# Optimization experiments

Hardware: AMD Instinct MI355X
Metric: run time of the kernel (lower is better)

## Reference

```python
import jax, jax.numpy as jnp
import numpy as np

B, N, DIN, U, K, DEG = 64, 512, 256, 128, 2, 8
BN = B * N
E = BN * DEG
D4 = 4 * U
HEADS = 2


def setup_inputs() -> dict:
    key = jax.random.key(0)
    ks = jax.random.split(key, 24)
    rng = np.random.default_rng(0)
    # block-diagonal batched graph: each of B graphs has N nodes, N*DEG random edges
    src = rng.integers(0, N, size=(B, N * DEG))
    dst = rng.integers(0, N, size=(B, N * DEG))
    off = (np.arange(B) * N)[:, None]
    edge_index = jnp.asarray(np.stack([(src + off).reshape(-1), (dst + off).reshape(-1)]), dtype=jnp.int32)

    def w(k, shape, fan):
        return (jax.random.normal(k, shape, dtype=jnp.float32) / np.sqrt(fan)).astype(jnp.float32)

    gin = (DIN + U) * (K + 1)  # gconv concatenates K+1 hop features of concat([x, h])
    inp = dict(
        x_od=jax.random.normal(ks[0], (BN, DIN), dtype=jnp.float32),
        history=jax.random.normal(ks[1], (BN, DIN), dtype=jnp.float32),
        yesterday=jax.random.normal(ks[2], (BN, DIN), dtype=jnp.float32),
        edge_index=edge_index,
        edge_weight=jax.random.uniform(ks[3], (E,), dtype=jnp.float32),
        W_ru_f=w(ks[4], (gin, 2 * U), gin), b_ru_f=jnp.zeros((2 * U,), jnp.float32),
        W_c_f=w(ks[5], (gin, U), gin), b_c_f=jnp.zeros((U,), jnp.float32),
        W_ru_l=w(ks[6], (gin, 2 * U), gin), b_ru_l=jnp.zeros((2 * U,), jnp.float32),
        W_c_l=w(ks[7], (gin, U), gin), b_c_l=jnp.zeros((U,), jnp.float32),
        W_ru_s=w(ks[8], (gin, 2 * U), gin), b_ru_s=jnp.zeros((2 * U,), jnp.float32),
        W_c_s=w(ks[9], (gin, U), gin), b_c_s=jnp.zeros((U,), jnp.float32),
        W_hd=w(ks[10], (D4, 2 * U), 2 * U), b_hd=jnp.zeros((D4,), jnp.float32),
        W_in=w(ks[11], (3 * D4, D4), D4), b_in=jnp.zeros((3 * D4,), jnp.float32),
        W_out=w(ks[12], (D4, D4), D4), b_out=jnp.zeros((D4,), jnp.float32),
        W_gate=w(ks[13], (U, D4), D4), b_gate=jnp.zeros((U,), jnp.float32),
    )
    return inp


def _gconv(x, src, dst, ew, W, b):
    # K-hop mean-normalized graph convolution over the batched edge list
    num = x.shape[0]
    deg = jnp.maximum(jax.ops.segment_sum(ew, dst, num_segments=num), 1.0)[:, None]
    feats = [x]
    h = x
    for _ in range(K):
        h = jax.ops.segment_sum(h[src] * ew[:, None], dst, num_segments=num) / deg
        feats.append(h)
    return jnp.concatenate(feats, axis=-1) @ W + b


def _ggru(x, h, src, dst, ew, W_ru, b_ru, W_c, b_c):
    ru = jax.nn.sigmoid(_gconv(jnp.concatenate([x, h], -1), src, dst, ew, W_ru, b_ru))
    r, u = jnp.split(ru, 2, axis=-1)
    c = jnp.tanh(_gconv(jnp.concatenate([x, r * h], -1), src, dst, ew, W_c, b_c))
    return u * h + (1.0 - u) * c


def _pos_enc(seq_len, d):
    pos = jnp.arange(seq_len, dtype=jnp.float32)[:, None]
    div = jnp.exp(jnp.arange(0, d, 2, dtype=jnp.float32) * (-jnp.log(10000.0) / d))
    pe = jnp.zeros((seq_len, d), jnp.float32)
    pe = pe.at[:, 0::2].set(jnp.sin(pos * div)).at[:, 1::2].set(jnp.cos(pos * div))
    return pe  # (seq_len, d)


def reference(x_od, history, yesterday, edge_index, edge_weight,
              W_ru_f, b_ru_f, W_c_f, b_c_f,
              W_ru_l, b_ru_l, W_c_l, b_c_l,
              W_ru_s, b_ru_s, W_c_s, b_c_s,
              W_hd, b_hd, W_in, b_in, W_out, b_out, W_gate, b_gate):
    src, dst = edge_index[0], edge_index[1]
    ew = edge_weight
    h0 = jnp.zeros((BN, U), jnp.float32)
    hf = _ggru(x_od, h0, src, dst, ew, W_ru_f, b_ru_f, W_c_f, b_c_f)      # finished branch
    hl = _ggru(history, h0, src, dst, ew, W_ru_l, b_ru_l, W_c_l, b_c_l)  # long-history branch
    hs = _ggru(yesterday, h0, src, dst, ew, W_ru_s, b_ru_s, W_c_s, b_c_s)  # short-history branch
    # hidden fusion: raw view(-1, 2U, N) as in the torch source
    fusion = jnp.concatenate([hs, hl], axis=-1).reshape(B, 2 * U, N)
    uh = jnp.einsum('oc,bcn->bon', W_hd, fusion) + b_hd[:, None]  # (B, 4U, N)
    uh = uh + _pos_enc(B, D4)[:, :, None]                          # pos-enc over batch dim, as in source
    x = uh.transpose(2, 0, 1)                                      # (N, B, 4U): seq=N, batch=B
    # multi-head self-attention (torch MultiheadAttention semantics)
    qkv = x @ W_in.T + b_in
    q, k_, v = jnp.split(qkv, 3, axis=-1)
    hd = D4 // HEADS
    qh = q.reshape(N, B, HEADS, hd)
    kh = k_.reshape(N, B, HEADS, hd)
    vh = v.reshape(N, B, HEADS, hd)
    scores = jnp.einsum('sbhd,tbhd->bhst', qh, kh) / jnp.sqrt(jnp.float32(hd))
    attn = jax.nn.softmax(scores, axis=-1)
    ctx = jnp.einsum('bhst,tbhd->sbhd', attn, vh).reshape(N, B, D4)
    attn_out = ctx @ W_out.T + b_out                               # (N, B, 4U)
    gated = jnp.einsum('oc,bcn->bon', W_gate, attn_out.transpose(1, 2, 0)) + b_gate[:, None]  # (B, U, N)
    attn_flat = gated.transpose(0, 2, 1).reshape(BN, U)
    # (enc_first_out==finished_hidden, long_hidden, short_hidden, gated attention)
    return jnp.stack([hf, hl, hs, attn_flat])
```

## Files before the change

### kernel.cpp

```cpp
#include <hip/hip_runtime.h>
#include <hip/hip_bf16.h>
#include <math.h>


#define DEV __device__ __forceinline__

typedef __attribute__((ext_vector_type(4))) float  f32x4;
typedef __attribute__((ext_vector_type(4))) float  fvec4;
typedef __attribute__((ext_vector_type(8))) short  bf16x8;
typedef __attribute__((ext_vector_type(4))) unsigned short u16x4;

constexpr int BN_ = 32768;
constexpr int E_  = 262144;
constexpr long OUTSEC = 4194304;
constexpr long ZSZE = 25165824;

DEV unsigned short f2bf(float f){
  union { float f; unsigned u; } v; v.f = f;
  unsigned r = (v.u + 0x7FFFu + ((v.u >> 16) & 1u)) >> 16;
  return (unsigned short)r;
}
DEV float b2f(unsigned short h){
  union { unsigned u; float f; } v; v.u = ((unsigned)h) << 16;
  return v.f;
}

__global__ __launch_bounds__(256) void histdeg_kernel(const int* __restrict__ ei,
    const float* __restrict__ ew, unsigned* __restrict__ cnt, float* __restrict__ deg){
  int e = blockIdx.x*256 + threadIdx.x;
  int d = ei[E_ + e];
  atomicAdd(&cnt[d], 1u);
  atomicAdd(&deg[d], ew[e]);
}

__global__ __launch_bounds__(1024) void scan_kernel(const unsigned* __restrict__ cnt,
                                                    unsigned* __restrict__ rowptr){
  __shared__ unsigned sm[1024];
  __shared__ unsigned carry;
  int tid = threadIdx.x;
  if (tid == 0) carry = 0;
  __syncthreads();
  for (int base = 0; base < BN_; base += 1024){
    unsigned v = cnt[base + tid];
    sm[tid] = v;
    __syncthreads();
    for (int off = 1; off < 1024; off <<= 1){
      unsigned t = (tid >= off) ? sm[tid - off] : 0u;
      __syncthreads();
      sm[tid] += t;
      __syncthreads();
    }
    rowptr[base + tid] = carry + sm[tid] - v;
    __syncthreads();
    if (tid == 1023) carry += sm[1023];
    __syncthreads();
  }
  if (tid == 0) rowptr[BN_] = carry;
}

__global__ __launch_bounds__(256) void scatter_kernel(const int* __restrict__ ei,
    const float* __restrict__ ew, const unsigned* __restrict__ rowptr,
    unsigned* __restrict__ curs, unsigned* __restrict__ csrc, float* __restrict__ csrw){
  int e = blockIdx.x*256 + threadIdx.x;
  int d = ei[E_ + e];
  unsigned pos = atomicAdd(&curs[d], 1u);
  unsigned idx = rowptr[d] + pos;
  csrc[idx] = (unsigned)ei[e];
  csrw[idx] = ew[e];
}

template<int SRC>
__global__ __launch_bounds__(256) void prop3_kernel(const float* __restrict__ x0,
    const float* __restrict__ x1, const float* __restrict__ x2,
    unsigned short* __restrict__ zcat,
    const unsigned* __restrict__ rowptr, const unsigned* __restrict__ csrc,
    const float* __restrict__ csrw, const float* __restrict__ deg){
  int node = blockIdx.x*4 + (threadIdx.x >> 6);
  int l = threadIdx.x & 63;
  int z = blockIdx.z;
  const float* xf = (z == 0) ? x0 : (z == 1) ? x1 : x2;
  const unsigned short* zin = zcat + z*ZSZE + 256;
  unsigned short* zout = zcat + z*ZSZE + (SRC == 0 ? 256 : 512);
  unsigned b0 = rowptr[node], b1 = rowptr[node + 1];
  float a0 = 0.f, a1 = 0.f, a2 = 0.f, a3 = 0.f;
  for (unsigned e = b0; e < b1; ++e){
    int s = csrc[e]; float w = csrw[e];
    if constexpr (SRC == 0){
      fvec4 v = *(const fvec4*)(xf + (long)s*256 + l*4);
      a0 += w*v[0]; a1 += w*v[1]; a2 += w*v[2]; a3 += w*v[3];
    } else {
      u16x4 v = *(const u16x4*)(zin + (long)s*768 + l*4);
      a0 += w*b2f(v[0]); a1 += w*b2f(v[1]); a2 += w*b2f(v[2]); a3 += w*b2f(v[3]);
    }
  }
  float dg = deg[node]; dg = dg > 1.f ? dg : 1.f;
  float inv = 1.f / dg;
  u16x4 o = { f2bf(a0*inv), f2bf(a1*inv), f2bf(a2*inv), f2bf(a3*inv) };
  *(u16x4*)(zout + (long)node*768 + l*4) = o;
}

__global__ __launch_bounds__(256) void convx3_kernel(const float* __restrict__ x0,
    const float* __restrict__ x1, const float* __restrict__ x2,
    unsigned short* __restrict__ zcat){
  int id = blockIdx.x*256 + threadIdx.x;
  int z = blockIdx.z;
  const float* xf = (z == 0) ? x0 : (z == 1) ? x1 : x2;
  fvec4 v = ((const fvec4*)xf)[id];
  int m = id >> 6, c4 = id & 63;
  u16x4 o = { f2bf(v[0]), f2bf(v[1]), f2bf(v[2]), f2bf(v[3]) };
  *(u16x4*)(zcat + z*ZSZE + (long)m*768 + c4*4) = o;
}

__global__ __launch_bounds__(256) void cvt_f2b_kernel(const float* __restrict__ s,
                                                      unsigned short* __restrict__ d, int n){
  int i = blockIdx.x*256 + threadIdx.x;
  if (i < n) d[i] = f2bf(s[i]);
}

__global__ __launch_bounds__(256) void tcvt_kernel(const float* __restrict__ s,
    unsigned short* __restrict__ d, int lgC, int R){
  int id = blockIdx.x*256 + threadIdx.x;
  int r = id >> lgC, c = id & ((1 << lgC) - 1);
  d[(long)c*R + r] = f2bf(s[id]);
}

__global__ __launch_bounds__(256) void weff3_kernel(
    const float* __restrict__ Wru0, const float* __restrict__ Wru1, const float* __restrict__ Wru2,
    const float* __restrict__ bru0, const float* __restrict__ bru1, const float* __restrict__ bru2,
    const float* __restrict__ Wc0,  const float* __restrict__ Wc1,  const float* __restrict__ Wc2,
    const float* __restrict__ bc0,  const float* __restrict__ bc1,  const float* __restrict__ bc2,
    unsigned short* __restrict__ Weff, float* __restrict__ beff){
  int z = blockIdx.y;
  const float* Wru = (z == 0) ? Wru0 : (z == 1) ? Wru1 : Wru2;
  const float* bru = (z == 0) ? bru0 : (z == 1) ? bru1 : bru2;
  const float* Wc  = (z == 0) ? Wc0  : (z == 1) ? Wc1  : Wc2;
  const float* bc  = (z == 0) ? bc0  : (z == 1) ? bc1  : bc2;
  int id = blockIdx.x*256 + threadIdx.x;
  int n = id / 768, k = id % 768;
  int row = (k >> 8)*384 + (k & 255);
  int j = n >> 1;
  float w = ((n & 1) == 0) ? Wru[(long)row*256 + 128 + j] : Wc[(long)row*128 + j];
  Weff[(long)z*196608 + (long)n*768 + k] = f2bf(w);
  if (k == 0) beff[z*256 + n] = ((n & 1) == 0) ? bru[128 + j] : bc[j];
}

__global__ __launch_bounds__(256) void pe_kernel(const float* __restrict__ bhd,
                                                 float* __restrict__ PET4){
  int id = blockIdx.x*256 + threadIdx.x;
  int b = id >> 9, o = id & 511;
  float j2 = (float)(o & ~1);
  float ang = (float)b * expf(-j2 * (9.210340371976184f / 512.f));
  float v = ((o & 1) ? cosf(ang) : sinf(ang)) + bhd[o];
  PET4[(o >> 2)*256 + b*4 + (o & 3)] = v;
}

__global__ __launch_bounds__(256) void peq2_kernel(const float* __restrict__ Win,
    const float* __restrict__ bin, const float* __restrict__ PET4, float* __restrict__ peq2){
  int j = blockIdx.x*4 + (threadIdx.x >> 6);
  int l = threadIdx.x & 63;
  float acc = 0.f;
  for (int o4 = 0; o4 < 128; ++o4){
    fvec4 wv = *(const fvec4*)(Win + (long)j*512 + o4*4);
    fvec4 pv = *(const fvec4*)(PET4 + o4*256 + l*4);
    acc += wv[0]*pv[0] + wv[1]*pv[1] + wv[2]*pv[2] + wv[3]*pv[3];
  }
  peq2[(long)l*1536 + j] = bin[j] + acc;
}

__global__ __launch_bounds__(128) void beq_kernel(const float* __restrict__ Wgt,
    const float* __restrict__ bout, const float* __restrict__ bgate, float* __restrict__ beq){
  int g = threadIdx.x;
  float s = bgate[g];
  for (int c = 0; c < 512; ++c) s += Wgt[(long)g*512 + c] * bout[c];
  beq[g] = s;
}

template<int MODE, int EPI>
__global__ __launch_bounds__(256) void gemm_bt(
    const unsigned short* __restrict__ A, const unsigned short* __restrict__ Bt,
    float* __restrict__ Cf, unsigned short* __restrict__ Cb,
    int Ktot, int lda, int ldb, int ldc,
    long sA, long sB, long sC, int g0,
    const float* __restrict__ bias, const float* __restrict__ pe, float scale)
{
  __shared__ unsigned short As[2][8192];
  __shared__ unsigned short Bs[2][8192];
  const int tid = threadIdx.x;
  long aOff, bOff, cOff;
  if constexpr (MODE == 0 || MODE == 3){
    aOff = blockIdx.z * sA; bOff = blockIdx.z * sB; cOff = blockIdx.z * sC;
  } else if constexpr (MODE == 1){
    int g = g0 + blockIdx.z;
    long base = (long)(g >> 1)*1536 + (long)(g & 1)*256;
    aOff = base; bOff = base + 512; cOff = (long)blockIdx.z * 262144;
  } else {
    int g = g0 + blockIdx.z;
    aOff = (long)blockIdx.z * 262144;
    bOff = (long)g * 131072;
    cOff = (long)g * 256;
  }
  const int bm = blockIdx.y * 128, bn = blockIdx.x * 128;
  const int w = tid >> 6, l = tid & 63;
  const int wr = w >> 1, wc = w & 1;

  const unsigned short* aB[4];
  const unsigned short* bB[4];
  #pragma unroll
  for (int i = 0; i < 4; ++i){
    int c = tid + i*256;
    int row = c >> 3, gg = c & 7;
    aB[i] = A  + aOff + (long)(bm + row)*lda + gg*8;
    bB[i] = Bt + bOff + (long)(bn + row)*ldb + gg*8;
  }

  f32x4 acc[4][4] = {};

  auto stage = [&](int p, int kt){
    #pragma unroll
    for (int i = 0; i < 4; ++i){
      __builtin_amdgcn_global_load_lds(
        (const __attribute__((address_space(1))) unsigned int*)(aB[i] + kt),
        (__attribute__((address_space(3))) unsigned int*)&As[p][(i*256 + w*64)*8], 16, 0, 0);
      __builtin_amdgcn_global_load_lds(
        (const __attribute__((address_space(1))) unsigned int*)(bB[i] + kt),
        (__attribute__((address_space(3))) unsigned int*)&Bs[p][(i*256 + w*64)*8], 16, 0, 0);
    }
  };
  auto compute = [&](int p){
    #pragma unroll
    for (int ks = 0; ks < 2; ++ks){
      bf16x8 aF[4], bF[4];
      #pragma unroll
      for (int mi = 0; mi < 4; ++mi)
        aF[mi] = *(const bf16x8*)(&As[p][(wr*64 + mi*16 + (l & 15))*64 + ks*32 + (l >> 4)*8]);
      #pragma unroll
      for (int ni = 0; ni < 4; ++ni)
        bF[ni] = *(const bf16x8*)(&Bs[p][(wc*64 + ni*16 + (l & 15))*64 + ks*32 + (l >> 4)*8]);
      #pragma unroll
      for (int mi = 0; mi < 4; ++mi)
        #pragma unroll
        for (int ni = 0; ni < 4; ++ni)
          acc[mi][ni] = __builtin_amdgcn_mfma_f32_16x16x32_bf16(aF[mi], bF[ni], acc[mi][ni], 0, 0, 0);
    }
  };

  const int nt = Ktot >> 6;
  stage(0, 0);
  __syncthreads();
  for (int t = 0; t < nt - 1; ++t){
    stage((t + 1) & 1, (t + 1) << 6);
    compute(t & 1);
    __syncthreads();
  }
  compute((nt - 1) & 1);

  #pragma unroll
  for (int mi = 0; mi < 4; ++mi){
    #pragma unroll
    for (int ni = 0; ni < 4; ++ni){
      int col = bn + wc*64 + ni*16 + (l & 15);
      int row0 = bm + wr*64 + mi*16 + ((l >> 4) << 2);
      #pragma unroll
      for (int j = 0; j < 4; ++j){
        int row = row0 + j;
        float v = acc[mi][ni][j] * scale;
        if (bias){
          if constexpr (MODE == 3) v += bias[(int)blockIdx.z*256 + col];
          else v += bias[col];
        }
        if constexpr (EPI == 5) v += pe[((row & 63) * 1536) + col];
        if constexpr (EPI == 0){
          Cf[cOff + (long)row*ldc + col] = v;
        } else if constexpr (EPI == 4){
          long orow = (long)(row & 63)*512 + (row >> 6);
          Cf[orow*ldc + col] = v;
        } else if constexpr (EPI == 7){
          float other = __shfl_xor(v, 1);
          if (!(l & 1)){
            float uu = 1.f / (1.f + expf(-v));
            Cf[cOff + (long)row*ldc + (col >> 1)] = (1.f - uu) * tanhf(other);
          }
        } else {
          Cb[cOff + (long)row*ldc + col] = f2bf(v);
        }
      }
    }
  }
}

__global__ __launch_bounds__(256) void afus_kernel(const float* __restrict__ out,
                                                   unsigned short* __restrict__ Afus){
  __shared__ float sm[64][132];
  int cq = blockIdx.x, a = blockIdx.y, b = blockIdx.z;
  int tid = threadIdx.x;
  #pragma unroll
  for (int half = 0; half < 2; ++half){
    const float* sec = out + (half ? 1 : 2)*OUTSEC;
    int cl = tid >> 2, r0 = (tid & 3)*4;
    long srow = ((long)b*512 + 2*(cq*64 + cl) + a)*128;
    #pragma unroll
    for (int it = 0; it < 8; ++it){
      int r = r0 + it*16;
      fvec4 v = *(const fvec4*)(sec + srow + r);
      *(fvec4*)&sm[cl][r] = v;
    }
    __syncthreads();
    int r = tid >> 1;
    int c0 = (tid & 1)*32;
    long mrow = ((long)a*256 + half*128 + r)*64 + b;
    unsigned short* dst = Afus + mrow*256 + cq*64 + c0;
    #pragma unroll
    for (int jj = 0; jj < 8; ++jj){
      int c = c0 + jj*4;
      u16x4 o = { f2bf(sm[c][r]), f2bf(sm[c+1][r]), f2bf(sm[c+2][r]), f2bf(sm[c+3][r]) };
      *(u16x4*)(dst + jj*4) = o;
    }
    __syncthreads();
  }
}

__global__ __launch_bounds__(256) void vt_kernel(const unsigned short* __restrict__ qkv,
                                                 unsigned short* __restrict__ vT){
  int g = blockIdx.y; int b = g >> 1, h = g & 1;
  int tt = blockIdx.x & 7, dt = blockIdx.x >> 3;
  __shared__ unsigned short sm[64][65];
  int lrow = threadIdx.x >> 6, lcol = threadIdx.x & 63;
  const unsigned short* src = qkv + (long)b*1536 + 1024 + (long)h*256 + dt*64;
  #pragma unroll
  for (int i = 0; i < 16; ++i){
    int t = tt*64 + lrow + i*4;
    sm[lrow + i*4][lcol] = src[(long)t*98304 + lcol];
  }
  __syncthreads();
  unsigned short* dstp = vT + (long)g*131072 + (long)(dt*64)*512 + tt*64;
  #pragma unroll
  for (int i = 0; i < 16; ++i){
    int d = lrow + i*4;
    dstp[(long)d*512 + lcol] = sm[lcol][d];
  }
}

__global__ __launch_bounds__(256) void smax_kernel(unsigned short* __restrict__ S){
  long row = (long)blockIdx.x*4 + (threadIdx.x >> 6);
  int l = threadIdx.x & 63;
  unsigned short* p = S + row*512 + l*8;
  bf16x8 v = *(const bf16x8*)p;
  float f[8];
  #pragma unroll
  for (int j = 0; j < 8; ++j) f[j] = b2f((unsigned short)v[j]);
  float m = f[0];
  #pragma unroll
  for (int j = 1; j < 8; ++j) m = fmaxf(m, f[j]);
  #pragma unroll
  for (int off = 32; off; off >>= 1) m = fmaxf(m, __shfl_xor(m, off));
  float s = 0.f;
  #pragma unroll
  for (int j = 0; j < 8; ++j){ f[j] = expf(f[j] - m); s += f[j]; }
  #pragma unroll
  for (int off = 32; off; off >>= 1) s += __shfl_xor(s, off);
  float inv = 1.f / s;
  bf16x8 o;
  #pragma unroll
  for (int j = 0; j < 8; ++j) o[j] = (short)f2bf(f[j]*inv);
  *(bf16x8*)p = o;
}

extern "C" void kernel_launch(void* const* d_in, const int* in_sizes, int n_in,
                              void* d_out, int out_size, void* d_ws, size_t ws_size,
                              hipStream_t stream)
{
  (void)in_sizes; (void)n_in; (void)out_size;
  constexpr long MB = 1l << 20;
  if (ws_size < 200*MB) return;

  const float* x0 = (const float*)d_in[0];
  const float* x1 = (const float*)d_in[1];
  const float* x2 = (const float*)d_in[2];
  const int*   ei = (const int*)d_in[3];
  const float* ew = (const float*)d_in[4];
  const float* Whd  = (const float*)d_in[17]; const float* bhd   = (const float*)d_in[18];
  const float* Win  = (const float*)d_in[19]; const float* bin   = (const float*)d_in[20];
  const float* Wout = (const float*)d_in[21]; const float* bout  = (const float*)d_in[22];
  const float* Wgt  = (const float*)d_in[23]; const float* bgate = (const float*)d_in[24];
  float* out = (float*)d_out;
  char* ws = (char*)d_ws;

  float*    deg    = (float*)(ws + 0);
  unsigned* cnt    = (unsigned*)(ws + 131072);
  unsigned* rowptr = (unsigned*)(ws + 262144);
  unsigned* curs   = (unsigned*)(ws + 524288);
  unsigned* csrc   = (unsigned*)(ws + 786432);
  float*    csrw   = (float*)(ws + 1835008);
  unsigned short* Weff = (unsigned short*)(ws + 2883584);
  float*    beff   = (float*)(ws + 4063232);
  float*    beq    = (float*)(ws + 4194304);
  unsigned short* WIN   = (unsigned short*)(ws + 4456448);
  unsigned short* WGTB  = (unsigned short*)(ws + 6029312);
  unsigned short* WHDT  = (unsigned short*)(ws + 6160384);
  unsigned short* WOUTT = (unsigned short*)(ws + 6422528);
  unsigned short* Wq2t  = (unsigned short*)(ws + 6946816);
  unsigned short* Weqt  = (unsigned short*)(ws + 7733248);
  float*    PET4   = (float*)(ws + 7864320);
  float*    PEQ2   = (float*)(ws + 7995392);
  unsigned short* ZCAT3 = (unsigned short*)(ws + 40*MB);
  unsigned short* AFUS  = (unsigned short*)(ws + 8*MB);
  unsigned short* QKV   = (unsigned short*)(ws + 40*MB);
  unsigned short* VT    = (unsigned short*)(ws + 8*MB);
  unsigned short* SCOREB= (unsigned short*)(ws + 136*MB);
  unsigned short* CTX   = (unsigned short*)(ws + 40*MB);

  hipMemsetAsync(deg,  0, 131072, stream);
  hipMemsetAsync(cnt,  0, 131072, stream);
  hipMemsetAsync(curs, 0, 131072, stream);
  histdeg_kernel<<<1024, 256, 0, stream>>>(ei, ew, cnt, deg);
  scan_kernel<<<1, 1024, 0, stream>>>(cnt, rowptr);
  scatter_kernel<<<1024, 256, 0, stream>>>(ei, ew, rowptr, curs, csrc, csrw);

  weff3_kernel<<<dim3(768,3), 256, 0, stream>>>(
      (const float*)d_in[5], (const float*)d_in[9],  (const float*)d_in[13],
      (const float*)d_in[6], (const float*)d_in[10], (const float*)d_in[14],
      (const float*)d_in[7], (const float*)d_in[11], (const float*)d_in[15],
      (const float*)d_in[8], (const float*)d_in[12], (const float*)d_in[16],
      Weff, beff);
  cvt_f2b_kernel<<<3072, 256, 0, stream>>>(Win, WIN,  786432);
  cvt_f2b_kernel<<<256,  256, 0, stream>>>(Wgt, WGTB, 65536);
  tcvt_kernel<<<512,  256, 0, stream>>>(Whd,  WHDT,  8, 512);
  tcvt_kernel<<<1024, 256, 0, stream>>>(Wout, WOUTT, 9, 512);
  pe_kernel<<<128, 256, 0, stream>>>(bhd, PET4);

  gemm_bt<0,2><<<dim3(2,12,1), 256, 0, stream>>>(WIN, WHDT, nullptr, Wq2t,
      512, 512, 512, 256, 0,0,0, 0, nullptr, nullptr, 1.0f);
  gemm_bt<0,2><<<dim3(4,1,1), 256, 0, stream>>>(WGTB, WOUTT, nullptr, Weqt,
      512, 512, 512, 512, 0,0,0, 0, nullptr, nullptr, 1.0f);
  peq2_kernel<<<384, 256, 0, stream>>>(Win, bin, PET4, PEQ2);
  beq_kernel<<<1, 128, 0, stream>>>(Wgt, bout, bgate, beq);

  convx3_kernel<<<dim3(8192,1,3), 256, 0, stream>>>(x0, x1, x2, ZCAT3);
  prop3_kernel<0><<<dim3(8192,1,3), 256, 0, stream>>>(x0, x1, x2, ZCAT3,
                                                      rowptr, csrc, csrw, deg);
  prop3_kernel<1><<<dim3(8192,1,3), 256, 0, stream>>>(x0, x1, x2, ZCAT3,
                                                      rowptr, csrc, csrw, deg);
  gemm_bt<3,7><<<dim3(2,256,3), 256, 0, stream>>>(ZCAT3, Weff, out, nullptr,
      768, 768, 768, 128, ZSZE, 196608, OUTSEC, 0, beff, nullptr, 1.0f);

  afus_kernel<<<dim3(4,2,64), 256, 0, stream>>>(out, AFUS);
  gemm_bt<0,5><<<dim3(12,256,1), 256, 0, stream>>>(AFUS, Wq2t, nullptr, QKV,
      256, 256, 256, 1536, 0,0,0, 0, nullptr, PEQ2, 1.0f);
  vt_kernel<<<dim3(32,128), 256, 0, stream>>>(QKV, VT);

  gemm_bt<1,2><<<dim3(4,4,128), 256, 0, stream>>>(QKV, QKV, nullptr, SCOREB,
      256, 98304, 98304, 512, 0,0,0, 0, nullptr, nullptr, 0.0625f);
  smax_kernel<<<16384, 256, 0, stream>>>(SCOREB);
  gemm_bt<2,2><<<dim3(2,4,128), 256, 0, stream>>>(SCOREB, VT, nullptr, CTX,
      512, 512, 512, 32768, 0,0,0, 0, nullptr, nullptr, 1.0f);

  gemm_bt<0,4><<<dim3(1,256,1), 256, 0, stream>>>(CTX, Weqt, out + 3*OUTSEC, nullptr,
      512, 512, 512, 128, 0,0,0, 0, beq, nullptr, 1.0f);
}
```

Before: 1.010 ms.

## Single-buffer GEMM LDS, add XCD block swizzle, unroll bf16 graph propagation

The GEMM now uses a single LDS buffer with a sync before and after compute instead of double buffering. This halves LDS use and may raise occupancy, but global-to-LDS loads no longer overlap with MFMA work. A block-ID swizzle groups workgroups in strides of eight, likely to match XCD placement for L2 locality. Hop-1 propagation now reads the bf16 copy in zcat instead of fp32 x, and the edge loop is unrolled by two. That halves gather bytes but adds bf16 rounding to the hop-1 inputs.

```diff
diff --git a/kernel.cpp b/kernel.cpp
--- a/kernel.cpp
+++ b/kernel.cpp
@@ -70,28 +70,31 @@
 }
 
 template<int SRC>
-__global__ __launch_bounds__(256) void prop3_kernel(const float* __restrict__ x0,
-    const float* __restrict__ x1, const float* __restrict__ x2,
-    unsigned short* __restrict__ zcat,
+__global__ __launch_bounds__(256) void prop3_kernel(unsigned short* __restrict__ zcat,
     const unsigned* __restrict__ rowptr, const unsigned* __restrict__ csrc,
     const float* __restrict__ csrw, const float* __restrict__ deg){
   int node = blockIdx.x*4 + (threadIdx.x >> 6);
   int l = threadIdx.x & 63;
   int z = blockIdx.z;
-  const float* xf = (z == 0) ? x0 : (z == 1) ? x1 : x2;
-  const unsigned short* zin = zcat + z*ZSZE + 256;
+  const unsigned short* zin = zcat + z*ZSZE + (SRC == 0 ? 0 : 256);
   unsigned short* zout = zcat + z*ZSZE + (SRC == 0 ? 256 : 512);
   unsigned b0 = rowptr[node], b1 = rowptr[node + 1];
   float a0 = 0.f, a1 = 0.f, a2 = 0.f, a3 = 0.f;
-  for (unsigned e = b0; e < b1; ++e){
+  unsigned e = b0;
+  for (; e + 2 <= b1; e += 2){
+    int s0 = csrc[e];     float w0 = csrw[e];
+    int s1 = csrc[e + 1]; float w1 = csrw[e + 1];
+    u16x4 v0 = *(const u16x4*)(zin + (long)s0*768 + l*4);
+    u16x4 v1 = *(const u16x4*)(zin + (long)s1*768 + l*4);
+    a0 += w0*b2f(v0[0]) + w1*b2f(v1[0]);
+    a1 += w0*b2f(v0[1]) + w1*b2f(v1[1]);
+    a2 += w0*b2f(v0[2]) + w1*b2f(v1[2]);
+    a3 += w0*b2f(v0[3]) + w1*b2f(v1[3]);
+  }
+  if (e < b1){
     int s = csrc[e]; float w = csrw[e];
-    if constexpr (SRC == 0){
-      fvec4 v = *(const fvec4*)(xf + (long)s*256 + l*4);
-      a0 += w*v[0]; a1 += w*v[1]; a2 += w*v[2]; a3 += w*v[3];
-    } else {
-      u16x4 v = *(const u16x4*)(zin + (long)s*768 + l*4);
-      a0 += w*b2f(v[0]); a1 += w*b2f(v[1]); a2 += w*b2f(v[2]); a3 += w*b2f(v[3]);
-    }
+    u16x4 v = *(const u16x4*)(zin + (long)s*768 + l*4);
+    a0 += w*b2f(v[0]); a1 += w*b2f(v[1]); a2 += w*b2f(v[2]); a3 += w*b2f(v[3]);
   }
   float dg = deg[node]; dg = dg > 1.f ? dg : 1.f;
   float inv = 1.f / dg;
@@ -175,7 +178,7 @@
   beq[g] = s;
 }
 
-template<int MODE, int EPI>
+template<int MODE, int EPI, int SWZ>
 __global__ __launch_bounds__(256) void gemm_bt(
     const unsigned short* __restrict__ A, const unsigned short* __restrict__ Bt,
     float* __restrict__ Cf, unsigned short* __restrict__ Cb,
@@ -183,23 +186,32 @@
     long sA, long sB, long sC, int g0,
     const float* __restrict__ bias, const float* __restrict__ pe, float scale)
 {
-  __shared__ unsigned short As[2][8192];
-  __shared__ unsigned short Bs[2][8192];
+  __shared__ unsigned short As[128*64];
+  __shared__ unsigned short Bs[128*64];
   const int tid = threadIdx.x;
+  int bx = blockIdx.x, by = blockIdx.y, bzi = blockIdx.z;
+  if constexpr (SWZ){
+    int gx = gridDim.x, gy = gridDim.y;
+    int nwg = gx*gy*(int)gridDim.z;
+    int wid = (bzi*gy + by)*gx + bx;
+    int swz = (wid & 7)*(nwg >> 3) + (wid >> 3);
+    bx = swz % gx; int rem = swz / gx;
+    by = rem % gy; bzi = rem / gy;
+  }
   long aOff, bOff, cOff;
   if constexpr (MODE == 0 || MODE == 3){
-    aOff = blockIdx.z * sA; bOff = blockIdx.z * sB; cOff = blockIdx.z * sC;
+    aOff = bzi * sA; bOff = bzi * sB; cOff = bzi * sC;
   } else if constexpr (MODE == 1){
-    int g = g0 + blockIdx.z;
+    int g = g0 + bzi;
     long base = (long)(g >> 1)*1536 + (long)(g & 1)*256;
-    aOff = base; bOff = base + 512; cOff = (long)blockIdx.z * 262144;
+    aOff = base; bOff = base + 512; cOff = (long)bzi * 262144;
   } else {
-    int g = g0 + blockIdx.z;
-    aOff = (long)blockIdx.z * 262144;
+    int g = g0 + bzi;
+    aOff = (long)bzi * 262144;
     bOff = (long)g * 131072;
     cOff = (long)g * 256;
   }
-  const int bm = blockIdx.y * 128, bn = blockIdx.x * 128;
+  const int bm = by * 128, bn = bx * 128;
   const int w = tid >> 6, l = tid & 63;
   const int wr = w >> 1, wc = w & 1;
 
@@ -214,46 +226,34 @@
   }
 
   f32x4 acc[4][4] = {};
-
-  auto stage = [&](int p, int kt){
+  for (int kt = 0; kt < Ktot; kt += 64){
     #pragma unroll
     for (int i = 0; i < 4; ++i){
       __builtin_amdgcn_global_load_lds(
         (const __attribute__((address_space(1))) unsigned int*)(aB[i] + kt),
-        (__attribute__((address_space(3))) unsigned int*)&As[p][(i*256 + w*64)*8], 16, 0, 0);
+        (__attribute__((address_space(3))) unsigned int*)&As[(i*256 + w*64)*8], 16, 0, 0);
       __builtin_amdgcn_global_load_lds(
         (const __attribute__((address_space(1))) unsigned int*)(bB[i] + kt),
-        (__attribute__((address_space(3))) unsigned int*)&Bs[p][(i*256 + w*64)*8], 16, 0, 0);
-    }
-  };
-  auto compute = [&](int p){
+        (__attribute__((address_space(3))) unsigned int*)&Bs[(i*256 + w*64)*8], 16, 0, 0);
+    }
+    __syncthreads();
     #pragma unroll
     for (int ks = 0; ks < 2; ++ks){
       bf16x8 aF[4], bF[4];
       #pragma unroll
       for (int mi = 0; mi < 4; ++mi)
-        aF[mi] = *(const bf16x8*)(&As[p][(wr*64 + mi*16 + (l & 15))*64 + ks*32 + (l >> 4)*8]);
+        aF[mi] = *(const bf16x8*)(&As[(wr*64 + mi*16 + (l & 15))*64 + ks*32 + (l >> 4)*8]);
       #pragma unroll
       for (int ni = 0; ni < 4; ++ni)
-        bF[ni] = *(const bf16x8*)(&Bs[p][(wc*64 + ni*16 + (l & 15))*64 + ks*32 + (l >> 4)*8]);
+        bF[ni] = *(const bf16x8*)(&Bs[(wc*64 + ni*16 + (l & 15))*64 + ks*32 + (l >> 4)*8]);
       #pragma unroll
       for (int mi = 0; mi < 4; ++mi)
         #pragma unroll
         for (int ni = 0; ni < 4; ++ni)
           acc[mi][ni] = __builtin_amdgcn_mfma_f32_16x16x32_bf16(aF[mi], bF[ni], acc[mi][ni], 0, 0, 0);
     }
-  };
-
-  const int nt = Ktot >> 6;
-  stage(0, 0);
-  __syncthreads();
-  for (int t = 0; t < nt - 1; ++t){
-    stage((t + 1) & 1, (t + 1) << 6);
-    compute(t & 1);
-    __syncthreads();
-  }
-  compute((nt - 1) & 1);
-
+    __syncthreads();
+  }
   #pragma unroll
   for (int mi = 0; mi < 4; ++mi){
     #pragma unroll
@@ -265,7 +265,7 @@
         int row = row0 + j;
         float v = acc[mi][ni][j] * scale;
         if (bias){
-          if constexpr (MODE == 3) v += bias[(int)blockIdx.z*256 + col];
+          if constexpr (MODE == 3) v += bias[bzi*256 + col];
           else v += bias[col];
         }
         if constexpr (EPI == 5) v += pe[((row & 63) * 1536) + col];
@@ -428,32 +428,30 @@
   tcvt_kernel<<<1024, 256, 0, stream>>>(Wout, WOUTT, 9, 512);
   pe_kernel<<<128, 256, 0, stream>>>(bhd, PET4);
 
-  gemm_bt<0,2><<<dim3(2,12,1), 256, 0, stream>>>(WIN, WHDT, nullptr, Wq2t,
+  gemm_bt<0,2,0><<<dim3(2,12,1), 256, 0, stream>>>(WIN, WHDT, nullptr, Wq2t,
       512, 512, 512, 256, 0,0,0, 0, nullptr, nullptr, 1.0f);
-  gemm_bt<0,2><<<dim3(4,1,1), 256, 0, stream>>>(WGTB, WOUTT, nullptr, Weqt,
+  gemm_bt<0,2,0><<<dim3(4,1,1), 256, 0, stream>>>(WGTB, WOUTT, nullptr, Weqt,
       512, 512, 512, 512, 0,0,0, 0, nullptr, nullptr, 1.0f);
   peq2_kernel<<<384, 256, 0, stream>>>(Win, bin, PET4, PEQ2);
   beq_kernel<<<1, 128, 0, stream>>>(Wgt, bout, bgate, beq);
 
   convx3_kernel<<<dim3(8192,1,3), 256, 0, stream>>>(x0, x1, x2, ZCAT3);
-  prop3_kernel<0><<<dim3(8192,1,3), 256, 0, stream>>>(x0, x1, x2, ZCAT3,
-                                                      rowptr, csrc, csrw, deg);
-  prop3_kernel<1><<<dim3(8192,1,3), 256, 0, stream>>>(x0, x1, x2, ZCAT3,
-                                                      rowptr, csrc, csrw, deg);
-  gemm_bt<3,7><<<dim3(2,256,3), 256, 0, stream>>>(ZCAT3, Weff, out, nullptr,
+  prop3_kernel<0><<<dim3(8192,1,3), 256, 0, stream>>>(ZCAT3, rowptr, csrc, csrw, deg);
+  prop3_kernel<1><<<dim3(8192,1,3), 256, 0, stream>>>(ZCAT3, rowptr, csrc, csrw, deg);
+  gemm_bt<3,7,1><<<dim3(2,256,3), 256, 0, stream>>>(ZCAT3, Weff, out, nullptr,
       768, 768, 768, 128, ZSZE, 196608, OUTSEC, 0, beff, nullptr, 1.0f);
 
   afus_kernel<<<dim3(4,2,64), 256, 0, stream>>>(out, AFUS);
-  gemm_bt<0,5><<<dim3(12,256,1), 256, 0, stream>>>(AFUS, Wq2t, nullptr, QKV,
+  gemm_bt<0,5,1><<<dim3(12,256,1), 256, 0, stream>>>(AFUS, Wq2t, nullptr, QKV,
       256, 256, 256, 1536, 0,0,0, 0, nullptr, PEQ2, 1.0f);
   vt_kernel<<<dim3(32,128), 256, 0, stream>>>(QKV, VT);
 
-  gemm_bt<1,2><<<dim3(4,4,128), 256, 0, stream>>>(QKV, QKV, nullptr, SCOREB,
+  gemm_bt<1,2,1><<<dim3(4,4,128), 256, 0, stream>>>(QKV, QKV, nullptr, SCOREB,
       256, 98304, 98304, 512, 0,0,0, 0, nullptr, nullptr, 0.0625f);
   smax_kernel<<<16384, 256, 0, stream>>>(SCOREB);
-  gemm_bt<2,2><<<dim3(2,4,128), 256, 0, stream>>>(SCOREB, VT, nullptr, CTX,
+  gemm_bt<2,2,1><<<dim3(2,4,128), 256, 0, stream>>>(SCOREB, VT, nullptr, CTX,
       512, 512, 512, 32768, 0,0,0, 0, nullptr, nullptr, 1.0f);
 
-  gemm_bt<0,4><<<dim3(1,256,1), 256, 0, stream>>>(CTX, Weqt, out + 3*OUTSEC, nullptr,
+  gemm_bt<0,4,1><<<dim3(1,256,1), 256, 0, stream>>>(CTX, Weqt, out + 3*OUTSEC, nullptr,
       512, 512, 512, 128, 0,0,0, 0, beq, nullptr, 1.0f);
 }
```

Measured after the change: 865.6 us. -14.3%, faster.
